# Optimization experiments

Hardware: AMD Instinct MI355X
Metric: run time of the kernel (lower is better)

## Reference

```python
import jax, jax.numpy as jnp
import numpy as np
from jax import lax

GAMMA = 0.99
TAU = 0.95
B = 4194304  # batchsz (flat trajectory length)


def setup_inputs() -> dict:
    key = jax.random.key(0)
    k_r, k_v, k_m = jax.random.split(key, 3)
    r = jax.random.normal(k_r, (B,), dtype=jnp.float32)
    v = jax.random.normal(k_v, (B,), dtype=jnp.float32)
    mask = jax.random.randint(k_m, (B,), 0, 2, dtype=jnp.int32)  # 0 = episode end
    return {"r": r, "v": v, "mask": mask}


def reference(r, v, mask):
    """GAE advantage + V-target via a reverse linear-recurrence scan.

    v_target[t] = r[t] + gamma * v_target[t+1] * mask[t]
    delta[t]    = r[t] + gamma * v[t+1]        * mask[t] - v[t]
    A_sa[t]     = delta[t] + gamma * tau * A_sa[t+1] * mask[t]
    A_sa normalized to zero mean / unit (unbiased) std, as in torch .std().
    """
    m = mask.astype(r.dtype)

    def step(carry, x):
        prev_vt, prev_v, prev_A = carry
        r_t, v_t, m_t = x
        vt = r_t + GAMMA * prev_vt * m_t
        delta = r_t + GAMMA * prev_v * m_t - v_t
        A = delta + GAMMA * TAU * prev_A * m_t
        return (vt, v_t, A), (vt, A)

    zero = jnp.float32(0.0)
    _, (v_target, A_sa) = lax.scan(step, (zero, zero, zero), (r, v, m), reverse=True)
    A_sa = (A_sa - A_sa.mean()) / jnp.std(A_sa, ddof=1)
    return A_sa, v_target
```

## Files before the change

kernel.cpp:

```cpp
#include <hip/hip_runtime.h>
#include <math.h>

#define BTOT 4194304
#define TPB  256
#define EPT  16
#define CS   (TPB * EPT)
#define NCH  (BTOT / CS)
#define CPT  (NCH / TPB)


__constant__ const float kG  = 0.99f;
__constant__ const float kGT = 0.99f * 0.95f;

__device__ __forceinline__ float wave_redf(float x) {
#pragma unroll
    for (int o = 32; o > 0; o >>= 1) x += __shfl_down(x, o);
    return x;
}
__device__ __forceinline__ double wave_redd(double x) {
#pragma unroll
    for (int o = 32; o > 0; o >>= 1) x += __shfl_down(x, o);
    return x;
}

__device__ __forceinline__ void block_suffix_scan(
    float pv, float sv, float pa, float sa,
    float* lpv, float* lsv, float* lpa, float* lsa, int j)
{
    lpv[j] = pv; lsv[j] = sv; lpa[j] = pa; lsa[j] = sa;
    __syncthreads();
#pragma unroll
    for (int d = 1; d < TPB; d <<= 1) {
        float cpv = lpv[j], csv = lsv[j], cpa = lpa[j], csa = lsa[j];
        bool has = (j + d) < TPB;
        float qpv = 1.0f, qsv = 0.0f, qpa = 1.0f, qsa = 0.0f;
        if (has) { qpv = lpv[j+d]; qsv = lsv[j+d]; qpa = lpa[j+d]; qsa = lsa[j+d]; }
        __syncthreads();
        if (has) {
            lpv[j] = cpv * qpv; lsv[j] = csv + cpv * qsv;
            lpa[j] = cpa * qpa; lsa[j] = csa + cpa * qsa;
        }
        __syncthreads();
    }
}

__global__ __launch_bounds__(TPB) void ppo_k1_summarize(
    const float* __restrict__ r, const float* __restrict__ v,
    const int* __restrict__ mk, float* __restrict__ ws) {
    const int c = blockIdx.x;
    const int j = threadIdx.x;
    const int base = c * CS + j * EPT;

    float rr[EPT], vv[EPT + 1], dd[EPT];
    int mm[EPT];
    const float4* r4 = (const float4*)(r + base);
    const float4* v4 = (const float4*)(v + base);
    const int4*   m4 = (const int4*)(mk + base);
#pragma unroll
    for (int k = 0; k < EPT / 4; ++k) {
        float4 a = r4[k];
        rr[4*k] = a.x; rr[4*k+1] = a.y; rr[4*k+2] = a.z; rr[4*k+3] = a.w;
        float4 b = v4[k];
        vv[4*k] = b.x; vv[4*k+1] = b.y; vv[4*k+2] = b.z; vv[4*k+3] = b.w;
        int4 m = m4[k];
        mm[4*k] = m.x; mm[4*k+1] = m.y; mm[4*k+2] = m.z; mm[4*k+3] = m.w;
    }
    vv[EPT] = (base + EPT < BTOT) ? v[base + EPT] : 0.0f;

#pragma unroll
    for (int k = 0; k < EPT; ++k) {
        float m = (float)mm[k];
        dd[k] = rr[k] + kG * m * vv[k + 1] - vv[k];
    }

    float pv = 1.0f, sv = 0.0f, pa = 1.0f, sa = 0.0f;
#pragma unroll
    for (int k = EPT - 1; k >= 0; --k) {
        float m = (float)mm[k];
        float av = kG * m, aa = kGT * m;
        sv = rr[k] + av * sv;
        sa = dd[k] + aa * sa;
        pv *= av; pa *= aa;
    }

    __shared__ float lpv[TPB], lsv[TPB], lpa[TPB], lsa[TPB];
    block_suffix_scan(pv, sv, pa, sa, lpv, lsv, lpa, lsa, j);

    float CinA = (j + 1 < TPB) ? lsa[j + 1] : 0.0f;
    float QrA  = (j + 1 < TPB) ? lpa[j + 1] : 1.0f;
    float chPv = lpv[0], chSv = lsv[0], chPa = lpa[0], chSa = lsa[0];

    float x = CinA, ql = 1.0f;
    float s0 = 0, s1 = 0, s2 = 0, s3 = 0, s4 = 0;
#pragma unroll
    for (int k = EPT - 1; k >= 0; --k) {
        float m = (float)mm[k];
        float aa = kGT * m;
        x = dd[k] + aa * x;
        ql *= aa;
        float q = ql * QrA;
        s0 += x; s1 += q; s2 += x * x; s3 += x * q; s4 += q * q;
    }
    s0 = wave_redf(s0); s1 = wave_redf(s1); s2 = wave_redf(s2);
    s3 = wave_redf(s3); s4 = wave_redf(s4);
    __shared__ float rb[4][5];
    int wid = j >> 6, ln = j & 63;
    if (ln == 0) { rb[wid][0]=s0; rb[wid][1]=s1; rb[wid][2]=s2; rb[wid][3]=s3; rb[wid][4]=s4; }
    __syncthreads();
    if (j == 0) {
        float t0=0,t1=0,t2=0,t3=0,t4=0;
        for (int w = 0; w < 4; ++w) { t0+=rb[w][0]; t1+=rb[w][1]; t2+=rb[w][2]; t3+=rb[w][3]; t4+=rb[w][4]; }
        ws[0*NCH+c] = chPv; ws[1*NCH+c] = chSv; ws[2*NCH+c] = chPa; ws[3*NCH+c] = chSa;
        ws[4*NCH+c] = t0;   ws[5*NCH+c] = t1;   ws[6*NCH+c] = t2;
        ws[7*NCH+c] = t3;   ws[8*NCH+c] = t4;
    }
}

__global__ __launch_bounds__(TPB) void ppo_k2_finalize(
    const float* __restrict__ r, const float* __restrict__ v,
    const int* __restrict__ mk, const float* __restrict__ ws,
    float* __restrict__ outA, float* __restrict__ outV)
{
    const int c = blockIdx.x;
    const int j = threadIdx.x;
    const int base = c * CS + j * EPT;

    __shared__ float lpv[TPB], lsv[TPB], lpa[TPB], lsa[TPB];
    __shared__ double rd[4][2];
    __shared__ float bcast[4];

    {
        float cpv[CPT], csv[CPT], cpa[CPT], csa[CPT];
        {
            float4 t;
            t = *(const float4*)(ws + 0*NCH + 4*j); cpv[0]=t.x; cpv[1]=t.y; cpv[2]=t.z; cpv[3]=t.w;
            t = *(const float4*)(ws + 1*NCH + 4*j); csv[0]=t.x; csv[1]=t.y; csv[2]=t.z; csv[3]=t.w;
            t = *(const float4*)(ws + 2*NCH + 4*j); cpa[0]=t.x; cpa[1]=t.y; cpa[2]=t.z; cpa[3]=t.w;
            t = *(const float4*)(ws + 3*NCH + 4*j); csa[0]=t.x; csa[1]=t.y; csa[2]=t.z; csa[3]=t.w;
        }
        float gpv = 1.0f, gsv = 0.0f, gpa = 1.0f, gsa = 0.0f;
#pragma unroll
        for (int i = CPT - 1; i >= 0; --i) {
            gsv = csv[i] + cpv[i] * gsv; gpv = cpv[i] * gpv;
            gsa = csa[i] + cpa[i] * gsa; gpa = cpa[i] * gpa;
        }

        block_suffix_scan(gpv, gsv, gpa, gsa, lpv, lsv, lpa, lsa, j);

        float Cv = (j + 1 < TPB) ? lsv[j + 1] : 0.0f;
        float Ca = (j + 1 < TPB) ? lsa[j + 1] : 0.0f;

        float sLv[CPT], sqv[CPT], sL2v[CPT], sLqv[CPT], sq2v[CPT];
        {
            float4 t;
            t = *(const float4*)(ws + 4*NCH + 4*j); sLv[0]=t.x;  sLv[1]=t.y;  sLv[2]=t.z;  sLv[3]=t.w;
            t = *(const float4*)(ws + 5*NCH + 4*j); sqv[0]=t.x;  sqv[1]=t.y;  sqv[2]=t.z;  sqv[3]=t.w;
            t = *(const float4*)(ws + 6*NCH + 4*j); sL2v[0]=t.x; sL2v[1]=t.y; sL2v[2]=t.z; sL2v[3]=t.w;
            t = *(const float4*)(ws + 7*NCH + 4*j); sLqv[0]=t.x; sLqv[1]=t.y; sLqv[2]=t.z; sLqv[3]=t.w;
            t = *(const float4*)(ws + 8*NCH + 4*j); sq2v[0]=t.x; sq2v[1]=t.y; sq2v[2]=t.z; sq2v[3]=t.w;
        }
        double dS = 0.0, dS2 = 0.0;
#pragma unroll
        for (int i = CPT - 1; i >= 0; --i) {
            int g = 4*j + i;
            if (g == c) { bcast[0] = Cv; bcast[1] = Ca; }
            dS  += (double)(sLv[i]  + Ca * sqv[i]);
            dS2 += (double)(sL2v[i] + 2.0f * Ca * sLqv[i] + Ca * Ca * sq2v[i]);
            Cv = csv[i] + cpv[i] * Cv;
            Ca = csa[i] + cpa[i] * Ca;
        }
        dS = wave_redd(dS); dS2 = wave_redd(dS2);
        int wid = j >> 6, ln = j & 63;
        if (ln == 0) { rd[wid][0] = dS; rd[wid][1] = dS2; }
        __syncthreads();
        if (j == 0) {
            double S  = rd[0][0] + rd[1][0] + rd[2][0] + rd[3][0];
            double S2 = rd[0][1] + rd[1][1] + rd[2][1] + rd[3][1];
            double n = (double)BTOT;
            double mean = S / n;
            double var = (S2 - S * mean) / (n - 1.0);
            bcast[2] = (float)mean;
            bcast[3] = (float)(1.0 / sqrt(var));
        }
        __syncthreads();
    }

    float rr[EPT], vv[EPT + 1], dd[EPT];
    int mm[EPT];
    const float4* r4 = (const float4*)(r + base);
    const float4* v4 = (const float4*)(v + base);
    const int4*   m4 = (const int4*)(mk + base);
#pragma unroll
    for (int k = 0; k < EPT / 4; ++k) {
        float4 a = r4[k];
        rr[4*k] = a.x; rr[4*k+1] = a.y; rr[4*k+2] = a.z; rr[4*k+3] = a.w;
        float4 b = v4[k];
        vv[4*k] = b.x; vv[4*k+1] = b.y; vv[4*k+2] = b.z; vv[4*k+3] = b.w;
        int4 m = m4[k];
        mm[4*k] = m.x; mm[4*k+1] = m.y; mm[4*k+2] = m.z; mm[4*k+3] = m.w;
    }
    vv[EPT] = (base + EPT < BTOT) ? v[base + EPT] : 0.0f;
#pragma unroll
    for (int k = 0; k < EPT; ++k) {
        float m = (float)mm[k];
        dd[k] = rr[k] + kG * m * vv[k + 1] - vv[k];
    }

    float pv = 1.0f, sv = 0.0f, pa = 1.0f, sa = 0.0f;
#pragma unroll
    for (int k = EPT - 1; k >= 0; --k) {
        float m = (float)mm[k];
        float av = kG * m, aa = kGT * m;
        sv = rr[k] + av * sv;
        sa = dd[k] + aa * sa;
        pv *= av; pa *= aa;
    }
    block_suffix_scan(pv, sv, pa, sa, lpv, lsv, lpa, lsa, j);

    float CinV = (j + 1 < TPB) ? lsv[j + 1] : 0.0f;
    float QrV  = (j + 1 < TPB) ? lpv[j + 1] : 1.0f;
    float CinA = (j + 1 < TPB) ? lsa[j + 1] : 0.0f;
    float QrA  = (j + 1 < TPB) ? lpa[j + 1] : 1.0f;

    const float Ccv  = bcast[0];
    const float Cca  = bcast[1];
    const float mean = bcast[2];
    const float inv  = bcast[3];

    float xv = CinV + QrV * Ccv;
    float xa = CinA + QrA * Cca;
    float oA[EPT], oV[EPT];
#pragma unroll
    for (int k = EPT - 1; k >= 0; --k) {
        float m = (float)mm[k];
        xv = rr[k] + kG  * m * xv;
        xa = dd[k] + kGT * m * xa;
        oV[k] = xv;
        oA[k] = (xa - mean) * inv;
    }
    float4* a4 = (float4*)(outA + base);
    float4* w4 = (float4*)(outV + base);
#pragma unroll
    for (int k = 0; k < EPT / 4; ++k) {
        a4[k] = make_float4(oA[4*k], oA[4*k+1], oA[4*k+2], oA[4*k+3]);
        w4[k] = make_float4(oV[4*k], oV[4*k+1], oV[4*k+2], oV[4*k+3]);
    }
}

extern "C" void kernel_launch(void* const* d_in, const int* in_sizes, int n_in,
                              void* d_out, int out_size, void* d_ws, size_t ws_size,
                              hipStream_t stream) {
    const float* r  = (const float*)d_in[0];
    const float* v  = (const float*)d_in[1];
    const int*   mk = (const int*)d_in[2];
    float* outA = (float*)d_out;
    float* outV = outA + BTOT;
    float* ws   = (float*)d_ws;

    hipLaunchKernelGGL(ppo_k1_summarize, dim3(NCH), dim3(TPB), 0, stream,
                       r, v, mk, ws);
    hipLaunchKernelGGL(ppo_k2_finalize, dim3(NCH), dim3(TPB), 0, stream,
                       r, v, mk, ws, outA, outV);
}
```

Measured before the change: 115.3 us.

## Replace shared-memory block suffix scan with wave-shuffle scan and nontemporal stores

Replaces the LDS-based Hillis-Steele block suffix scan, which needs two barriers per step over eight steps, with a wave-level shuffle scan plus a small four-wave combine through shared memory. Each thread now gets its exclusive suffix and the block total directly in registers. The finalize kernel also writes its outputs per float4 group as it computes them, using nontemporal stores to avoid polluting the cache. Barrier placement changes, and the order of reads and writes to bcast now relies on the barriers inside the new scan helper.

```diff
diff --git a/kernel.cpp b/kernel.cpp
--- a/kernel.cpp
+++ b/kernel.cpp
@@ -12,6 +12,8 @@
 __constant__ const float kG  = 0.99f;
 __constant__ const float kGT = 0.99f * 0.95f;
 
+typedef float f4v __attribute__((ext_vector_type(4)));
+
 __device__ __forceinline__ float wave_redf(float x) {
 #pragma unroll
     for (int o = 32; o > 0; o >>= 1) x += __shfl_down(x, o);
@@ -23,25 +25,43 @@
     return x;
 }
 
-__device__ __forceinline__ void block_suffix_scan(
-    float pv, float sv, float pa, float sa,
-    float* lpv, float* lsv, float* lpa, float* lsa, int j)
+__device__ __forceinline__ void block_suffix_affine(
+    float pv, float sv, float pa, float sa, int j,
+    float& cpv, float& csv, float& cpa, float& csa,
+    float& tpv, float& tsv, float& tpa, float& tsa)
 {
-    lpv[j] = pv; lsv[j] = sv; lpa[j] = pa; lsa[j] = sa;
-    __syncthreads();
-#pragma unroll
-    for (int d = 1; d < TPB; d <<= 1) {
-        float cpv = lpv[j], csv = lsv[j], cpa = lpa[j], csa = lsa[j];
-        bool has = (j + d) < TPB;
-        float qpv = 1.0f, qsv = 0.0f, qpa = 1.0f, qsa = 0.0f;
-        if (has) { qpv = lpv[j+d]; qsv = lsv[j+d]; qpa = lpa[j+d]; qsa = lsa[j+d]; }
-        __syncthreads();
-        if (has) {
-            lpv[j] = cpv * qpv; lsv[j] = csv + cpv * qsv;
-            lpa[j] = cpa * qpa; lsa[j] = csa + cpa * qsa;
-        }
-        __syncthreads();
-    }
+    const int ln = j & 63, w = j >> 6;
+    __shared__ float wt[4][4];
+    __syncthreads();
+
+#pragma unroll
+    for (int o = 1; o < 64; o <<= 1) {
+        float qpv = __shfl_down(pv, o), qsv = __shfl_down(sv, o);
+        float qpa = __shfl_down(pa, o), qsa = __shfl_down(sa, o);
+        if (ln + o < 64) { sv += pv * qsv; pv *= qpv; sa += pa * qsa; pa *= qpa; }
+    }
+    float epv = __shfl_down(pv, 1), esv = __shfl_down(sv, 1);
+    float epa = __shfl_down(pa, 1), esa = __shfl_down(sa, 1);
+    if (ln == 63) { epv = 1.f; esv = 0.f; epa = 1.f; esa = 0.f; }
+
+    if (ln == 0) { wt[w][0] = pv; wt[w][1] = sv; wt[w][2] = pa; wt[w][3] = sa; }
+    __syncthreads();
+
+    float rpv = 1.f, rsv = 0.f, rpa = 1.f, rsa = 0.f;
+    for (int u = 3; u > w; --u) {
+        rsv = wt[u][1] + wt[u][0] * rsv; rpv = wt[u][0] * rpv;
+        rsa = wt[u][3] + wt[u][2] * rsa; rpa = wt[u][2] * rpa;
+    }
+    csv = esv + epv * rsv; cpv = epv * rpv;
+    csa = esa + epa * rsa; cpa = epa * rpa;
+
+    float t0pv = 1.f, t0sv = 0.f, t0pa = 1.f, t0sa = 0.f;
+#pragma unroll
+    for (int u = 3; u >= 0; --u) {
+        t0sv = wt[u][1] + wt[u][0] * t0sv; t0pv = wt[u][0] * t0pv;
+        t0sa = wt[u][3] + wt[u][2] * t0sa; t0pa = wt[u][2] * t0pa;
+    }
+    tpv = t0pv; tsv = t0sv; tpa = t0pa; tsa = t0sa;
 }
 
 __global__ __launch_bounds__(TPB) void ppo_k1_summarize(
@@ -83,12 +103,9 @@
         pv *= av; pa *= aa;
     }
 
-    __shared__ float lpv[TPB], lsv[TPB], lpa[TPB], lsa[TPB];
-    block_suffix_scan(pv, sv, pa, sa, lpv, lsv, lpa, lsa, j);
-
-    float CinA = (j + 1 < TPB) ? lsa[j + 1] : 0.0f;
-    float QrA  = (j + 1 < TPB) ? lpa[j + 1] : 1.0f;
-    float chPv = lpv[0], chSv = lsv[0], chPa = lpa[0], chSa = lsa[0];
+    float QrV, CinV, QrA, CinA, chPv, chSv, chPa, chSa;
+    block_suffix_affine(pv, sv, pa, sa, j,
+                        QrV, CinV, QrA, CinA, chPv, chSv, chPa, chSa);
 
     float x = CinA, ql = 1.0f;
     float s0 = 0, s1 = 0, s2 = 0, s3 = 0, s4 = 0;
@@ -125,7 +142,6 @@
     const int j = threadIdx.x;
     const int base = c * CS + j * EPT;
 
-    __shared__ float lpv[TPB], lsv[TPB], lpa[TPB], lsa[TPB];
     __shared__ double rd[4][2];
     __shared__ float bcast[4];
 
@@ -145,10 +161,9 @@
             gsa = csa[i] + cpa[i] * gsa; gpa = cpa[i] * gpa;
         }
 
-        block_suffix_scan(gpv, gsv, gpa, gsa, lpv, lsv, lpa, lsa, j);
-
-        float Cv = (j + 1 < TPB) ? lsv[j + 1] : 0.0f;
-        float Ca = (j + 1 < TPB) ? lsa[j + 1] : 0.0f;
+        float Qv_, Cv, Qa_, Ca, d0, d1, d2, d3;
+        block_suffix_affine(gpv, gsv, gpa, gsa, j,
+                            Qv_, Cv, Qa_, Ca, d0, d1, d2, d3);
 
         float sLv[CPT], sqv[CPT], sL2v[CPT], sLqv[CPT], sq2v[CPT];
         {
@@ -182,7 +197,6 @@
             bcast[2] = (float)mean;
             bcast[3] = (float)(1.0 / sqrt(var));
         }
-        __syncthreads();
     }
 
     float rr[EPT], vv[EPT + 1], dd[EPT];
@@ -215,12 +229,10 @@
         sa = dd[k] + aa * sa;
         pv *= av; pa *= aa;
     }
-    block_suffix_scan(pv, sv, pa, sa, lpv, lsv, lpa, lsa, j);
-
-    float CinV = (j + 1 < TPB) ? lsv[j + 1] : 0.0f;
-    float QrV  = (j + 1 < TPB) ? lpv[j + 1] : 1.0f;
-    float CinA = (j + 1 < TPB) ? lsa[j + 1] : 0.0f;
-    float QrA  = (j + 1 < TPB) ? lpa[j + 1] : 1.0f;
+    float QrV, CinV, QrA, CinA, u0, u1, u2, u3;
+    block_suffix_affine(pv, sv, pa, sa, j,
+                        QrV, CinV, QrA, CinA, u0, u1, u2, u3);
+    __syncthreads();
 
     const float Ccv  = bcast[0];
     const float Cca  = bcast[1];
@@ -229,21 +241,24 @@
 
     float xv = CinV + QrV * Ccv;
     float xa = CinA + QrA * Cca;
-    float oA[EPT], oV[EPT];
-#pragma unroll
-    for (int k = EPT - 1; k >= 0; --k) {
-        float m = (float)mm[k];
-        xv = rr[k] + kG  * m * xv;
-        xa = dd[k] + kGT * m * xa;
-        oV[k] = xv;
-        oA[k] = (xa - mean) * inv;
-    }
-    float4* a4 = (float4*)(outA + base);
-    float4* w4 = (float4*)(outV + base);
-#pragma unroll
-    for (int k = 0; k < EPT / 4; ++k) {
-        a4[k] = make_float4(oA[4*k], oA[4*k+1], oA[4*k+2], oA[4*k+3]);
-        w4[k] = make_float4(oV[4*k], oV[4*k+1], oV[4*k+2], oV[4*k+3]);
+    f4v* a4 = (f4v*)(outA + base);
+    f4v* w4 = (f4v*)(outV + base);
+#pragma unroll
+    for (int g = EPT/4 - 1; g >= 0; --g) {
+        float oa[4], ov[4];
+#pragma unroll
+        for (int k = 3; k >= 0; --k) {
+            int idx = 4*g + k;
+            float m = (float)mm[idx];
+            xv = rr[idx] + kG  * m * xv;
+            xa = dd[idx] + kGT * m * xa;
+            ov[k] = xv;
+            oa[k] = (xa - mean) * inv;
+        }
+        f4v va = { oa[0], oa[1], oa[2], oa[3] };
+        f4v vw = { ov[0], ov[1], ov[2], ov[3] };
+        __builtin_nontemporal_store(va, a4 + g);
+        __builtin_nontemporal_store(vw, w4 + g);
     }
 }
 
```

Result: slower. 153.4 us (+33.1%).
